# Kernel tuning notes

Measured on AMD Instinct MI355X. Metric: run time of the kernel, lower is better.

Reference implementation:

```python
import jax, jax.numpy as jnp
import numpy as np

BIAS = 7  # FP8 E4M3 exponent bias


def _decode(bits):
    # bits [..., 8] in order [s, e3, e2, e1, e0, m2, m1, m0]
    b = bits.astype(jnp.int32)
    s = b[..., 0]
    e = (b[..., 1] << 3) | (b[..., 2] << 2) | (b[..., 3] << 1) | b[..., 4]
    m = (b[..., 5] << 2) | (b[..., 6] << 1) | b[..., 7]
    return s, e, m


def _rne_rshift(M, sh):
    # round-to-nearest-even right shift of non-negative int M by sh (sh >= 0)
    q = M >> sh
    rem = M - (q << sh)
    half = jnp.right_shift(jnp.left_shift(1, sh), 1)  # 2^(sh-1), 0 when sh==0
    up = ((rem > half) | ((rem == half) & ((q & 1) == 1))) & (sh > 0)
    return q + up.astype(jnp.int32)


def setup_inputs() -> dict:
    key = jax.random.key(0)
    ks = jax.random.split(key, 6)
    shape = (1024, 4096)

    def make(k1, k2, k3):
        s = jax.random.randint(k1, shape, 0, 2)
        e = jax.random.randint(k2, shape, 0, 15)  # exclude e=15 (NaN region) for well-defined inputs
        m = jax.random.randint(k3, shape, 0, 8)
        bits = jnp.stack([s, (e >> 3) & 1, (e >> 2) & 1, (e >> 1) & 1, e & 1,
                          (m >> 2) & 1, (m >> 1) & 1, m & 1], axis=-1)
        return bits.astype(jnp.float32)

    return {"a": make(ks[0], ks[1], ks[2]), "b": make(ks[3], ks[4], ks[5])}


def _fp8_mul(a, b):
    sa, ea, ma = _decode(a)
    sb, eb_, mb = _decode(b)
    # significand with implicit bit; subnormals (e==0) use leading-zero-normalized form,
    # identical math to the module's mux_a_leading / shift_calc path
    sig_a = jnp.where(ea == 0, ma, ma + 8)
    sig_b = jnp.where(eb_ == 0, mb, mb + 8)
    exa = jnp.where(ea == 0, 1, ea) - BIAS
    exb = jnp.where(eb_ == 0, 1, eb_) - BIAS
    M = sig_a * sig_b              # exact 8-bit product, <= 225 (the 4x4 array multiplier)
    E = exa + exb - 6              # value = M * 2^E  (each sig in units of 2^-3)
    # MSB position p of M (M in [1, 225] => p in [0, 7])
    p = sum(((M >= (1 << k)).astype(jnp.int32) for k in range(1, 8)), start=jnp.zeros_like(M))
    eb_out = E + p + BIAS          # candidate biased exponent (normalization unit)
    # ---- normal path (eb_out >= 1): RNE round to 3 mantissa bits ----
    sh = p - 3
    shp = jnp.maximum(sh, 0)
    lsh = jnp.maximum(-sh, 0)
    mant4 = jnp.left_shift(_rne_rshift(M, shp), lsh)  # in [8, 16]
    carry = mant4 >> 4                                # rounding overflow -> exp += 1
    mant4 = jnp.where(mant4 == 16, 8, mant4)
    e_n = eb_out + carry
    m_n = mant4 - 8
    nan = e_n >= 16                                   # exponent overflow -> NaN (e=1111, m=111)
    e_n = jnp.where(nan, 15, e_n)
    m_n = jnp.where(nan, 7, m_n)
    # ---- subnormal path (eb_out <= 0): mant = RNE(M * 2^(E+9)), value = mant * 2^-9 ----
    t = E + 9
    mant_s = jnp.left_shift(_rne_rshift(M, jnp.clip(-t, 0, 30)), jnp.maximum(t, 0))
    e_s = jnp.where(mant_s >= 8, 1, 0)                # rounding promoted to smallest normal
    m_s = jnp.where(mant_s >= 8, 0, mant_s)
    # ---- select ----
    is_sub = eb_out <= 0
    e_o = jnp.where(is_sub, e_s, e_n)
    m_o = jnp.where(is_sub, m_s, m_n)
    zero = M == 0                                     # either input true zero
    e_o = jnp.where(zero, 0, e_o)
    m_o = jnp.where(zero, 0, m_o)
    s_o = sa ^ sb
    bits = jnp.stack([s_o, (e_o >> 3) & 1, (e_o >> 2) & 1, (e_o >> 1) & 1, e_o & 1,
                      (m_o >> 2) & 1, (m_o >> 1) & 1, m_o & 1], axis=-1)
    return bits.astype(jnp.float32)


def reference(a, b):
    return _fp8_mul(a, b)
```

## Files before the change

### kernel.cpp

```cpp
#include <hip/hip_runtime.h>


#define BIAS 7

__device__ __forceinline__ int rne_rshift(int M, int sh) {
    int q = M >> sh;
    int rem = M - (q << sh);
    int half = (1 << sh) >> 1;
    int up = ((rem > half) | ((rem == half) & (q & 1))) & (sh > 0);
    return q + up;
}

__device__ __forceinline__ int fp8_mul_byte(int a8, int b8) {
    int sa = a8 >> 7,        sb_ = b8 >> 7;
    int ea = (a8 >> 3) & 15, eb = (b8 >> 3) & 15;
    int ma = a8 & 7,         mb = b8 & 7;

    int sig_a = (ea == 0) ? ma : (ma + 8);
    int sig_b = (eb == 0) ? mb : (mb + 8);
    int exa = ((ea == 0) ? 1 : ea) - BIAS;
    int exb = ((eb == 0) ? 1 : eb) - BIAS;

    int M = sig_a * sig_b;
    int E = exa + exb - 6;

    int p = (M > 0) ? (31 - __clz(M)) : 0;
    int eb_out = E + p + BIAS;

    int sh  = p - 3;
    int shp = (sh > 0) ? sh : 0;
    int lsh = (sh < 0) ? -sh : 0;
    int mant4 = rne_rshift(M, shp) << lsh;
    int carry = mant4 >> 4;
    if (mant4 == 16) mant4 = 8;
    int e_n = eb_out + carry;
    int m_n = mant4 - 8;
    if (e_n >= 16) { e_n = 15; m_n = 7; }

    int t = E + 9;
    int rsh   = (-t < 0) ? 0 : ((-t > 30) ? 30 : -t);
    int lsh_s = (t > 0) ? t : 0;
    int mant_s = rne_rshift(M, rsh) << lsh_s;
    int e_s = (mant_s >= 8) ? 1 : 0;
    int m_s = (mant_s >= 8) ? 0 : mant_s;

    int is_sub = (eb_out <= 0);
    int e_o = is_sub ? e_s : e_n;
    int m_o = is_sub ? m_s : m_n;
    if (M == 0) { e_o = 0; m_o = 0; }
    int s_o = sa ^ sb_;
    return (s_o << 7) | (e_o << 3) | m_o;
}

__global__ void __launch_bounds__(256)
fp8_mul_kernel(const uint4* __restrict__ a, const uint4* __restrict__ b,
               float4* __restrict__ out, int n_vec) {
    int j = blockIdx.x * blockDim.x + threadIdx.x;
    if (j >= n_vec) return;

    uint4 av = a[j];
    uint4 bv = b[j];

    int na = ((av.x != 0) << 3) | ((av.y != 0) << 2) | ((av.z != 0) << 1) | (int)(av.w != 0);
    int nb = ((bv.x != 0) << 3) | ((bv.y != 0) << 2) | ((bv.z != 0) << 1) | (int)(bv.w != 0);
    int own = na | (nb << 4);
    int pp  = __shfl_xor(own, 1);

    int odd = j & 1;
    int a8 = odd ? (((pp  & 0xF) << 4) |  (own & 0xF))
                 : (((own & 0xF) << 4) |  (pp  & 0xF));
    int b8 = odd ? ((((pp  >> 4) & 0xF) << 4) | ((own >> 4) & 0xF))
                 : ((((own >> 4) & 0xF) << 4) | ((pp  >> 4) & 0xF));

    int r = fp8_mul_byte(a8, b8);

    int sbit = odd ? 3 : 7;
    float4 o;
    o.x = (float)((r >> sbit)       & 1);
    o.y = (float)((r >> (sbit - 1)) & 1);
    o.z = (float)((r >> (sbit - 2)) & 1);
    o.w = (float)((r >> (sbit - 3)) & 1);
    out[j] = o;
}

extern "C" void kernel_launch(void* const* d_in, const int* in_sizes, int n_in,
                              void* d_out, int out_size, void* d_ws, size_t ws_size,
                              hipStream_t stream) {
    const uint4* a = (const uint4*)d_in[0];
    const uint4* b = (const uint4*)d_in[1];
    float4* out = (float4*)d_out;
    int n_vec = in_sizes[0] / 4;
    int block = 256;
    int grid = (n_vec + block - 1) / block;
    fp8_mul_kernel<<<grid, block, 0, stream>>>(a, b, out, n_vec);
}
```

Before: 299.7 us.

## Process four vectors per thread with nontemporal stores and DPP lane swap

Each thread now handles four float4 groups, issuing all loads before any compute so more memory requests are in flight. The shuffle is replaced by a DPP quad-permute swap, bit extraction uses the float exponent bit instead of compare-to-zero, and stores are nontemporal. It relies on pairs of lanes being adjacent, which holds since odd is derived from threadIdx.x, and it assumes the inputs are exactly 0.0 or 1.0.

New measurement: 315.3 us. +5.2%, slower.

```diff
diff --git a/kernel.cpp b/kernel.cpp
--- a/kernel.cpp
+++ b/kernel.cpp
@@ -2,6 +2,9 @@
 
 
 #define BIAS 7
+#define KPT 4
+
+typedef float vfloat4 __attribute__((ext_vector_type(4)));
 
 __device__ __forceinline__ int rne_rshift(int M, int sh) {
     int q = M >> sh;
@@ -52,35 +55,61 @@
     return (s_o << 7) | (e_o << 3) | m_o;
 }
 
-__global__ void __launch_bounds__(256)
-fp8_mul_kernel(const uint4* __restrict__ a, const uint4* __restrict__ b,
-               float4* __restrict__ out, int n_vec) {
-    int j = blockIdx.x * blockDim.x + threadIdx.x;
-    if (j >= n_vec) return;
+__device__ __forceinline__ int compact_own(uint4 av, uint4 bv) {
+    return (int)(((av.x >> 20) & 8u)   | ((av.y >> 21) & 4u)  |
+                 ((av.z >> 22) & 2u)   | ((av.w >> 23) & 1u)  |
+                 ((bv.x >> 16) & 128u) | ((bv.y >> 17) & 64u) |
+                 ((bv.z >> 18) & 32u)  | ((bv.w >> 19) & 16u));
+}
 
-    uint4 av = a[j];
-    uint4 bv = b[j];
+__device__ __forceinline__ void compute_store(int own, int odd, int sbit,
+                                              vfloat4* __restrict__ dst) {
+    int pp = __builtin_amdgcn_update_dpp(0, own, 0xB1, 0xF, 0xF, true);
 
-    int na = ((av.x != 0) << 3) | ((av.y != 0) << 2) | ((av.z != 0) << 1) | (int)(av.w != 0);
-    int nb = ((bv.x != 0) << 3) | ((bv.y != 0) << 2) | ((bv.z != 0) << 1) | (int)(bv.w != 0);
-    int own = na | (nb << 4);
-    int pp  = __shfl_xor(own, 1);
-
-    int odd = j & 1;
-    int a8 = odd ? (((pp  & 0xF) << 4) |  (own & 0xF))
-                 : (((own & 0xF) << 4) |  (pp  & 0xF));
+    int a8 = odd ? (((pp  & 0xF) << 4)        |  (own & 0xF))
+                 : (((own & 0xF) << 4)        |  (pp  & 0xF));
     int b8 = odd ? ((((pp  >> 4) & 0xF) << 4) | ((own >> 4) & 0xF))
                  : ((((own >> 4) & 0xF) << 4) | ((pp  >> 4) & 0xF));
 
     int r = fp8_mul_byte(a8, b8);
 
-    int sbit = odd ? 3 : 7;
-    float4 o;
+    vfloat4 o;
     o.x = (float)((r >> sbit)       & 1);
     o.y = (float)((r >> (sbit - 1)) & 1);
     o.z = (float)((r >> (sbit - 2)) & 1);
     o.w = (float)((r >> (sbit - 3)) & 1);
-    out[j] = o;
+    __builtin_nontemporal_store(o, dst);
+}
+
+__global__ void __launch_bounds__(256)
+fp8_mul_kernel(const uint4* __restrict__ a, const uint4* __restrict__ b,
+               vfloat4* __restrict__ out, int n_vec) {
+    const int base = blockIdx.x * (256 * KPT) + threadIdx.x;
+    const int odd  = threadIdx.x & 1;
+    const int sbit = odd ? 3 : 7;
+
+    if (base + 256 * (KPT - 1) < n_vec) {
+        uint4 av[KPT], bv[KPT];
+#pragma unroll
+        for (int k = 0; k < KPT; ++k) {
+            av[k] = a[base + 256 * k];
+            bv[k] = b[base + 256 * k];
+        }
+        int own[KPT];
+#pragma unroll
+        for (int k = 0; k < KPT; ++k) own[k] = compact_own(av[k], bv[k]);
+#pragma unroll
+        for (int k = 0; k < KPT; ++k)
+            compute_store(own[k], odd, sbit, &out[base + 256 * k]);
+    } else {
+        for (int k = 0; k < KPT; ++k) {
+            int j = base + 256 * k;
+            if (j >= n_vec) continue;
+            uint4 av = a[j];
+            uint4 bv = b[j];
+            compute_store(compact_own(av, bv), odd, sbit, &out[j]);
+        }
+    }
 }
 
 extern "C" void kernel_launch(void* const* d_in, const int* in_sizes, int n_in,
@@ -88,9 +117,9 @@
                               hipStream_t stream) {
     const uint4* a = (const uint4*)d_in[0];
     const uint4* b = (const uint4*)d_in[1];
-    float4* out = (float4*)d_out;
+    vfloat4* out = (vfloat4*)d_out;
     int n_vec = in_sizes[0] / 4;
     int block = 256;
-    int grid = (n_vec + block - 1) / block;
+    int grid = (n_vec + block * KPT - 1) / (block * KPT);
     fp8_mul_kernel<<<grid, block, 0, stream>>>(a, b, out, n_vec);
 }
```
